# Kernel optimization log

Measured on AMD Instinct MI355X. Metric: run time of the kernel, lower is better.

The kernel has to match this reference:

```python
import jax, jax.numpy as jnp
import numpy as np

KERNEL = (3, 3, 3)
STRIDE = (1, 1, 1)
PAD = (1, 1, 1)
DIL = (1, 1, 1)


def _deform_unfold_3d(x, offset):
    # x: [B, C, D, H, W]; offset: [B, 3*K, Do, Ho, Wo] with per-tap (dd, dh, dw) order.
    B, C, D, H, W = x.shape
    kd, kh, kw = KERNEL
    K = kd * kh * kw
    Do = (D + 2 * PAD[0] - (DIL[0] * (kd - 1) + 1)) // STRIDE[0] + 1
    Ho = (H + 2 * PAD[1] - (DIL[1] * (kh - 1) + 1)) // STRIDE[1] + 1
    Wo = (W + 2 * PAD[2] - (DIL[2] * (kw - 1) + 1)) // STRIDE[2] + 1
    P = Do * Ho * Wo
    dt = x.dtype
    # kernel-tap base displacements, flattened to [K]
    ki, kj, kk = jnp.meshgrid(jnp.arange(kd), jnp.arange(kh), jnp.arange(kw), indexing="ij")
    bd = (ki.reshape(-1) * DIL[0] - PAD[0]).astype(dt)
    bh = (kj.reshape(-1) * DIL[1] - PAD[1]).astype(dt)
    bw = (kk.reshape(-1) * DIL[2] - PAD[2]).astype(dt)
    # output-grid anchor positions, flattened to [P]
    od, oh, ow = jnp.meshgrid(jnp.arange(Do), jnp.arange(Ho), jnp.arange(Wo), indexing="ij")
    gd = (od.reshape(-1) * STRIDE[0]).astype(dt)
    gh = (oh.reshape(-1) * STRIDE[1]).astype(dt)
    gw = (ow.reshape(-1) * STRIDE[2]).astype(dt)
    off = offset.reshape(B, K, 3, P)
    # sampling positions [B, K, P]
    pd = bd[None, :, None] + gd[None, None, :] + off[:, :, 0]
    ph = bh[None, :, None] + gh[None, None, :] + off[:, :, 1]
    pw = bw[None, :, None] + gw[None, None, :] + off[:, :, 2]
    d0f = jnp.floor(pd); fd = pd - d0f; d0 = d0f.astype(jnp.int32)
    h0f = jnp.floor(ph); fh = ph - h0f; h0 = h0f.astype(jnp.int32)
    w0f = jnp.floor(pw); fw = pw - w0f; w0 = w0f.astype(jnp.int32)
    xflat = x.reshape(B, C, D * H * W)
    out = jnp.zeros((B, C, K, P), dt)
    for ci in (0, 1):
        dsel = d0 + ci
        wd = (1.0 - fd) if ci == 0 else fd
        for cj in (0, 1):
            hsel = h0 + cj
            wh = (1.0 - fh) if cj == 0 else fh
            for ck in (0, 1):
                wsel = w0 + ck
                ww = (1.0 - fw) if ck == 0 else fw
                valid = (dsel >= 0) & (dsel < D) & (hsel >= 0) & (hsel < H) & (wsel >= 0) & (wsel < W)
                idx = (jnp.clip(dsel, 0, D - 1) * H + jnp.clip(hsel, 0, H - 1)) * W + jnp.clip(wsel, 0, W - 1)
                wgt = jnp.where(valid, wd * wh * ww, jnp.zeros((), dt))  # [B, K, P]
                val = jnp.take_along_axis(xflat, idx.reshape(B, 1, K * P), axis=2).reshape(B, C, K, P)
                out = out + wgt[:, None] * val
    return out.reshape(B, C * K, P)  # im2col columns, channel-major then kernel tap


def setup_inputs() -> dict:
    key = jax.random.key(0)
    k1, k2 = jax.random.split(key)
    inp = jax.random.normal(k1, (2, 16, 24, 48, 48), dtype=jnp.float32)
    offset = jax.random.normal(k2, (2, 81, 24, 48, 48), dtype=jnp.float32)
    return {"input": inp, "offset": offset}


def reference(input, offset):
    return _deform_unfold_3d(input, offset)
```

## Files before the change

### kernel.cpp

```cpp
#include <hip/hip_runtime.h>
#include <hip/hip_bf16.h>

typedef float f4 __attribute__((ext_vector_type(4)));
typedef float f2 __attribute__((ext_vector_type(2)));
typedef unsigned int u32;
typedef u32 u4 __attribute__((ext_vector_type(4)));

constexpr int B = 2, C = 16, D = 24, H = 48, W = 48;
constexpr int K = 27;
constexpr int SP = D * H * W;
constexpr int HW = H * W;

__device__ inline ushort bf16_bits(float f) {
    __hip_bfloat16 h = __float2bfloat16(f);
    return __builtin_bit_cast(ushort, h);
}

__global__ __launch_bounds__(256) void xpose_bf16_kernel(const float* __restrict__ x,
                                                         u32* __restrict__ xt) {
    int t = blockIdx.x * blockDim.x + threadIdx.x;
    if (t >= B * SP) return;
    int s = t % SP, b = t / SP;
    const float* src = x + (size_t)b * C * SP + s;
    u4 pk[2];
#pragma unroll
    for (int m = 0; m < 8; ++m) {
        float lo = src[(size_t)(2 * m) * SP];
        float hi = src[(size_t)(2 * m + 1) * SP];
        pk[m >> 2][m & 3] = (u32)bf16_bits(lo) | ((u32)bf16_bits(hi) << 16);
    }
    u4* dst = reinterpret_cast<u4*>(xt + (size_t)t * 8);
    dst[0] = pk[0];
    dst[1] = pk[1];
}

__global__ __launch_bounds__(256, 4) void deform_bf16_v9(const u32* __restrict__ xt,
                                                         const float* __restrict__ off,
                                                         float* __restrict__ out) {
    const int tid = blockIdx.x * blockDim.x + threadIdx.x;
    const int l = threadIdx.x & 63;
    const int q = l >> 5;
    const int c = l & 31;
    const int s = (tid >> 6) * 32 + c;
    const int p = s % SP;
    const int bk = s / SP;
    const int k = bk % K, b = bk / K;

    const size_t obase = ((size_t)b * (3 * K) + 3 * k) * SP;
    float vdh = __builtin_nontemporal_load(off + obase + (size_t)q * SP + p);
    float vw = 0.0f;
    if (l < 32) vw = __builtin_nontemporal_load(off + obase + (size_t)2 * SP + p);
    float offd = __shfl(vdh, c);
    float offh = __shfl(vdh, c + 32);
    float offw = __shfl(vw, c);

    const int od = p / HW;
    const int rem = p - od * HW;
    const int oh = rem / W, ow = rem - oh * W;
    const int ki = k / 9, kr2 = k - ki * 9;
    const int kj = kr2 / 3, kk = kr2 - kj * 3;

    float pd = (float)(od + ki - 1) + offd;
    float ph = (float)(oh + kj - 1) + offh;
    float pw = (float)(ow + kk - 1) + offw;

    float d0f = floorf(pd), h0f = floorf(ph), w0f = floorf(pw);
    float fd = pd - d0f, fh = ph - h0f, fw = pw - w0f;
    int d0 = (int)d0f, h0 = (int)h0f, w0 = (int)w0f;

    int dc0 = min(max(d0, 0), D - 1) * HW;
    int dc1 = min(max(d0 + 1, 0), D - 1) * HW;
    int hc0 = min(max(h0, 0), H - 1) * W;
    int hc1 = min(max(h0 + 1, 0), H - 1) * W;
    int wc0 = min(max(w0, 0), W - 1);
    int wc1 = min(max(w0 + 1, 0), W - 1);

    const u4* xb = reinterpret_cast<const u4*>(xt) + (size_t)b * SP * 2 + q;

    u4 v[8];
#pragma unroll
    for (int cn = 0; cn < 8; ++cn) {
        int idx = ((cn & 4) ? dc1 : dc0) + ((cn & 2) ? hc1 : hc0) + ((cn & 1) ? wc1 : wc0);
        v[cn] = xb[(size_t)idx * 2];
    }

    bool vd0 = (d0 >= 0) & (d0 < D), vd1 = (d0 + 1 >= 0) & (d0 + 1 < D);
    bool vh0 = (h0 >= 0) & (h0 < H), vh1 = (h0 + 1 >= 0) & (h0 + 1 < H);
    bool vw0 = (w0 >= 0) & (w0 < W), vw1 = (w0 + 1 >= 0) & (w0 + 1 < W);
    float wd0 = 1.0f - fd, wd1 = fd;
    float wh0 = 1.0f - fh, wh1 = fh;
    float ww0 = 1.0f - fw, ww1 = fw;

    float wgt[8];
#pragma unroll
    for (int cn = 0; cn < 8; ++cn) {
        bool valid = ((cn & 4) ? vd1 : vd0) & ((cn & 2) ? vh1 : vh0) & ((cn & 1) ? vw1 : vw0);
        float wv2 = ((cn & 4) ? wd1 : wd0) * ((cn & 2) ? wh1 : wh0) * ((cn & 1) ? ww1 : ww0);
        wgt[cn] = valid ? wv2 : 0.0f;
    }

    f2 acc[4] = {};
#pragma unroll
    for (int cn = 0; cn < 8; ++cn) {
        f2 w2 = {wgt[cn], wgt[cn]};
#pragma unroll
        for (int m = 0; m < 4; ++m) {
            u32 wb = v[cn][m];
            f2 xv = {__builtin_bit_cast(float, wb << 16),
                     __builtin_bit_cast(float, wb & 0xffff0000u)};
            acc[m] += w2 * xv;
        }
    }

    __shared__ float tile[4][16][36];
    const int wv = threadIdx.x >> 6;
#pragma unroll
    for (int m = 0; m < 4; ++m) {
        tile[wv][8 * q + 2 * m][c] = acc[m][0];
        tile[wv][8 * q + 2 * m + 1][c] = acc[m][1];
    }
    __syncthreads();

    const int p_base = p - c;
    const int ch_lo = l >> 3;
    const int p0 = 4 * (l & 7);
    float* osb = out + ((size_t)b * C * K) * SP + p_base + p0;
#pragma unroll
    for (int rr = 0; rr < 2; ++rr) {
        int ch = 8 * rr + ch_lo;
        f4 vv = *reinterpret_cast<const f4*>(&tile[wv][ch][p0]);
        *reinterpret_cast<f4*>(osb + ((size_t)ch * K + k) * SP) = vv;
    }
}

__global__ __launch_bounds__(256) void deform_kernel_nat(const float* __restrict__ x,
                                                         const float* __restrict__ off,
                                                         float* __restrict__ out) {
    int tid = blockIdx.x * blockDim.x + threadIdx.x;
    if (tid >= B * K * SP) return;
    int p = tid % SP;
    int bk = tid / SP;
    int k = bk % K, b = bk / K;

    const float* ob = off + ((size_t)b * (3 * K) + 3 * k) * SP + p;
    float offd = ob[0];
    float offh = ob[(size_t)SP];
    float offw = ob[(size_t)2 * SP];

    int od = p / HW, rem = p - od * HW;
    int oh = rem / W, ow = rem - oh * W;
    int ki = k / 9, kr = k - ki * 9;
    int kj = kr / 3, kk = kr - kj * 3;

    float pd = (float)(od + ki - 1) + offd;
    float ph = (float)(oh + kj - 1) + offh;
    float pw = (float)(ow + kk - 1) + offw;

    float d0f = floorf(pd), h0f = floorf(ph), w0f = floorf(pw);
    float fd = pd - d0f, fh = ph - h0f, fw = pw - w0f;
    int d0 = (int)d0f, h0 = (int)h0f, w0 = (int)w0f;

    f4 acc[4] = {};
#pragma unroll
    for (int ci = 0; ci < 2; ++ci) {
        int ds = d0 + ci;
        bool vd = (ds >= 0) & (ds < D);
        float wd = ci ? fd : 1.0f - fd;
        int dc = min(max(ds, 0), D - 1);
#pragma unroll
        for (int cj = 0; cj < 2; ++cj) {
            int hs = h0 + cj;
            bool vh = (hs >= 0) & (hs < H);
            float wh = cj ? fh : 1.0f - fh;
            int hc = min(max(hs, 0), H - 1);
#pragma unroll
            for (int ck = 0; ck < 2; ++ck) {
                int ws = w0 + ck;
                bool vw = (ws >= 0) & (ws < W);
                float ww = ck ? fw : 1.0f - fw;
                int wc = min(max(ws, 0), W - 1);
                float wgt = (vd & vh & vw) ? wd * wh * ww : 0.0f;
                int idx = (dc * H + hc) * W + wc;
                const float* src = x + (size_t)b * C * SP + idx;
#pragma unroll
                for (int c2 = 0; c2 < C; ++c2)
                    acc[c2 >> 2][c2 & 3] += wgt * src[(size_t)c2 * SP];
            }
        }
    }

    float* o = out + ((size_t)b * C * K + k) * SP + p;
#pragma unroll
    for (int c2 = 0; c2 < C; ++c2)
        o[(size_t)c2 * K * SP] = acc[c2 >> 2][c2 & 3];
}

extern "C" void kernel_launch(void* const* d_in, const int* in_sizes, int n_in,
                              void* d_out, int out_size, void* d_ws, size_t ws_size,
                              hipStream_t stream) {
    const float* x = (const float*)d_in[0];
    const float* off = (const float*)d_in[1];
    float* out = (float*)d_out;

    const size_t xt_bytes = (size_t)B * SP * 16 * sizeof(ushort);

    if (ws_size >= xt_bytes) {
        u32* xt = (u32*)d_ws;
        const int n_x = B * SP;
        xpose_bf16_kernel<<<(n_x + 255) / 256, 256, 0, stream>>>(x, xt);
        const long long n_thr = (long long)B * K * SP * 2;
        const int grid = (int)(n_thr / 256);
        deform_bf16_v9<<<grid, 256, 0, stream>>>(xt, off, out);
    } else {
        const int n_main = B * K * SP;
        deform_kernel_nat<<<(n_main + 255) / 256, 256, 0, stream>>>(x, off, out);
    }
}
```

Measured before the change: 106.2 us.

## Process two 32-point groups per wave and swizzle block order across XCDs

```diff
diff --git a/kernel.cpp b/kernel.cpp
--- a/kernel.cpp
+++ b/kernel.cpp
@@ -34,101 +34,112 @@
     dst[1] = pk[1];
 }
 
-__global__ __launch_bounds__(256, 4) void deform_bf16_v9(const u32* __restrict__ xt,
-                                                         const float* __restrict__ off,
-                                                         float* __restrict__ out) {
-    const int tid = blockIdx.x * blockDim.x + threadIdx.x;
+__global__ __launch_bounds__(256, 4) void deform_bf16_v11(const u32* __restrict__ xt,
+                                                          const float* __restrict__ off,
+                                                          float* __restrict__ out) {
+    const int cpx = gridDim.x >> 3;
+    const int sbid = (blockIdx.x & 7) * cpx + (blockIdx.x >> 3);
+    const int tid = sbid * 256 + threadIdx.x;
+
     const int l = threadIdx.x & 63;
     const int q = l >> 5;
     const int c = l & 31;
-    const int s = (tid >> 6) * 32 + c;
-    const int p = s % SP;
-    const int bk = s / SP;
-    const int k = bk % K, b = bk / K;
-
-    const size_t obase = ((size_t)b * (3 * K) + 3 * k) * SP;
-    float vdh = __builtin_nontemporal_load(off + obase + (size_t)q * SP + p);
-    float vw = 0.0f;
-    if (l < 32) vw = __builtin_nontemporal_load(off + obase + (size_t)2 * SP + p);
-    float offd = __shfl(vdh, c);
-    float offh = __shfl(vdh, c + 32);
-    float offw = __shfl(vw, c);
-
-    const int od = p / HW;
-    const int rem = p - od * HW;
-    const int oh = rem / W, ow = rem - oh * W;
+    const int w = tid >> 6;
+    const int plane = (w * 64) / SP;
+    const int p_base = (w * 64) % SP;
+    const int k = plane % K, b = plane / K;
+
     const int ki = k / 9, kr2 = k - ki * 9;
     const int kj = kr2 / 3, kk = kr2 - kj * 3;
 
-    float pd = (float)(od + ki - 1) + offd;
-    float ph = (float)(oh + kj - 1) + offh;
-    float pw = (float)(ow + kk - 1) + offw;
-
-    float d0f = floorf(pd), h0f = floorf(ph), w0f = floorf(pw);
-    float fd = pd - d0f, fh = ph - h0f, fw = pw - w0f;
-    int d0 = (int)d0f, h0 = (int)h0f, w0 = (int)w0f;
-
-    int dc0 = min(max(d0, 0), D - 1) * HW;
-    int dc1 = min(max(d0 + 1, 0), D - 1) * HW;
-    int hc0 = min(max(h0, 0), H - 1) * W;
-    int hc1 = min(max(h0 + 1, 0), H - 1) * W;
-    int wc0 = min(max(w0, 0), W - 1);
-    int wc1 = min(max(w0 + 1, 0), W - 1);
+    const size_t obase = ((size_t)b * (3 * K) + 3 * k) * SP + p_base;
+    float r0 = __builtin_nontemporal_load(off + obase + l);
+    float r1 = __builtin_nontemporal_load(off + obase + (size_t)SP + l);
+    float r2 = __builtin_nontemporal_load(off + obase + (size_t)2 * SP + l);
 
     const u4* xb = reinterpret_cast<const u4*>(xt) + (size_t)b * SP * 2 + q;
 
-    u4 v[8];
-#pragma unroll
-    for (int cn = 0; cn < 8; ++cn) {
-        int idx = ((cn & 4) ? dc1 : dc0) + ((cn & 2) ? hc1 : hc0) + ((cn & 1) ? wc1 : wc0);
-        v[cn] = xb[(size_t)idx * 2];
-    }
-
-    bool vd0 = (d0 >= 0) & (d0 < D), vd1 = (d0 + 1 >= 0) & (d0 + 1 < D);
-    bool vh0 = (h0 >= 0) & (h0 < H), vh1 = (h0 + 1 >= 0) & (h0 + 1 < H);
-    bool vw0 = (w0 >= 0) & (w0 < W), vw1 = (w0 + 1 >= 0) & (w0 + 1 < W);
-    float wd0 = 1.0f - fd, wd1 = fd;
-    float wh0 = 1.0f - fh, wh1 = fh;
-    float ww0 = 1.0f - fw, ww1 = fw;
-
-    float wgt[8];
-#pragma unroll
-    for (int cn = 0; cn < 8; ++cn) {
-        bool valid = ((cn & 4) ? vd1 : vd0) & ((cn & 2) ? vh1 : vh0) & ((cn & 1) ? vw1 : vw0);
-        float wv2 = ((cn & 4) ? wd1 : wd0) * ((cn & 2) ? wh1 : wh0) * ((cn & 1) ? ww1 : ww0);
-        wgt[cn] = valid ? wv2 : 0.0f;
-    }
-
-    f2 acc[4] = {};
-#pragma unroll
-    for (int cn = 0; cn < 8; ++cn) {
-        f2 w2 = {wgt[cn], wgt[cn]};
+    u4 v[2][8];
+    float wgt[2][8];
+#pragma unroll
+    for (int s2 = 0; s2 < 2; ++s2) {
+        const int p = p_base + 32 * s2 + c;
+        const float offd = __shfl(r0, 32 * s2 + c);
+        const float offh = __shfl(r1, 32 * s2 + c);
+        const float offw = __shfl(r2, 32 * s2 + c);
+
+        const int od = p / HW;
+        const int rem = p - od * HW;
+        const int oh = rem / W, ow = rem - oh * W;
+
+        float pd = (float)(od + ki - 1) + offd;
+        float ph = (float)(oh + kj - 1) + offh;
+        float pw = (float)(ow + kk - 1) + offw;
+
+        float d0f = floorf(pd), h0f = floorf(ph), w0f = floorf(pw);
+        float fd = pd - d0f, fh = ph - h0f, fw = pw - w0f;
+        int d0 = (int)d0f, h0 = (int)h0f, w0 = (int)w0f;
+
+        int dc0 = min(max(d0, 0), D - 1) * HW;
+        int dc1 = min(max(d0 + 1, 0), D - 1) * HW;
+        int hc0 = min(max(h0, 0), H - 1) * W;
+        int hc1 = min(max(h0 + 1, 0), H - 1) * W;
+        int wc0 = min(max(w0, 0), W - 1);
+        int wc1 = min(max(w0 + 1, 0), W - 1);
+
+#pragma unroll
+        for (int cn = 0; cn < 8; ++cn) {
+            int idx = ((cn & 4) ? dc1 : dc0) + ((cn & 2) ? hc1 : hc0) + ((cn & 1) ? wc1 : wc0);
+            v[s2][cn] = xb[(size_t)idx * 2];
+        }
+
+        bool vd0 = (d0 >= 0) & (d0 < D), vd1 = (d0 + 1 >= 0) & (d0 + 1 < D);
+        bool vh0 = (h0 >= 0) & (h0 < H), vh1 = (h0 + 1 >= 0) & (h0 + 1 < H);
+        bool vw0 = (w0 >= 0) & (w0 < W), vw1 = (w0 + 1 >= 0) & (w0 + 1 < W);
+        float wd0 = 1.0f - fd, wd1 = fd;
+        float wh0 = 1.0f - fh, wh1 = fh;
+        float ww0 = 1.0f - fw, ww1 = fw;
+#pragma unroll
+        for (int cn = 0; cn < 8; ++cn) {
+            bool valid = ((cn & 4) ? vd1 : vd0) & ((cn & 2) ? vh1 : vh0) & ((cn & 1) ? vw1 : vw0);
+            float ww2 = ((cn & 4) ? wd1 : wd0) * ((cn & 2) ? wh1 : wh0) * ((cn & 1) ? ww1 : ww0);
+            wgt[s2][cn] = valid ? ww2 : 0.0f;
+        }
+    }
+
+    f2 acc[2][4] = {};
+#pragma unroll
+    for (int s2 = 0; s2 < 2; ++s2)
+#pragma unroll
+        for (int cn = 0; cn < 8; ++cn) {
+            f2 w2 = {wgt[s2][cn], wgt[s2][cn]};
+#pragma unroll
+            for (int m = 0; m < 4; ++m) {
+                u32 wb = v[s2][cn][m];
+                f2 xv = {__builtin_bit_cast(float, wb << 16),
+                         __builtin_bit_cast(float, wb & 0xffff0000u)};
+                acc[s2][m] += w2 * xv;
+            }
+        }
+
+    __shared__ float tile[4][16][68];
+    const int wv = threadIdx.x >> 6;
+#pragma unroll
+    for (int s2 = 0; s2 < 2; ++s2)
 #pragma unroll
         for (int m = 0; m < 4; ++m) {
-            u32 wb = v[cn][m];
-            f2 xv = {__builtin_bit_cast(float, wb << 16),
-                     __builtin_bit_cast(float, wb & 0xffff0000u)};
-            acc[m] += w2 * xv;
-        }
-    }
-
-    __shared__ float tile[4][16][36];
-    const int wv = threadIdx.x >> 6;
-#pragma unroll
-    for (int m = 0; m < 4; ++m) {
-        tile[wv][8 * q + 2 * m][c] = acc[m][0];
-        tile[wv][8 * q + 2 * m + 1][c] = acc[m][1];
-    }
+            tile[wv][8 * q + 2 * m][32 * s2 + c] = acc[s2][m][0];
+            tile[wv][8 * q + 2 * m + 1][32 * s2 + c] = acc[s2][m][1];
+        }
     __syncthreads();
 
-    const int p_base = p - c;
-    const int ch_lo = l >> 3;
-    const int p0 = 4 * (l & 7);
-    float* osb = out + ((size_t)b * C * K) * SP + p_base + p0;
-#pragma unroll
-    for (int rr = 0; rr < 2; ++rr) {
-        int ch = 8 * rr + ch_lo;
-        f4 vv = *reinterpret_cast<const f4*>(&tile[wv][ch][p0]);
+    const int col = 4 * (l & 15);
+    const int ch_base = l >> 4;
+    float* osb = out + ((size_t)b * C * K) * SP + p_base + col;
+#pragma unroll
+    for (int j = 0; j < 4; ++j) {
+        int ch = 4 * j + ch_base;
+        f4 vv = *reinterpret_cast<const f4*>(&tile[wv][ch][col]);
         *reinterpret_cast<f4*>(osb + ((size_t)ch * K + k) * SP) = vv;
     }
 }
@@ -208,9 +219,9 @@
         u32* xt = (u32*)d_ws;
         const int n_x = B * SP;
         xpose_bf16_kernel<<<(n_x + 255) / 256, 256, 0, stream>>>(x, xt);
-        const long long n_thr = (long long)B * K * SP * 2;
+        const long long n_thr = (long long)B * K * SP;
         const int grid = (int)(n_thr / 256);
-        deform_bf16_v9<<<grid, 256, 0, stream>>>(xt, off, out);
+        deform_bf16_v11<<<grid, 256, 0, stream>>>(xt, off, out);
     } else {
         const int n_main = B * K * SP;
         deform_kernel_nat<<<(n_main + 255) / 256, 256, 0, stream>>>(x, off, out);
```

After: 119.6 us. 1.13x slower.
